# Performance work log

Hardware: AMD Instinct MI355X
Metric: run time of the kernel (lower is better)

Reference implementation:

```python
import jax, jax.numpy as jnp
import numpy as np

K = 50  # top-k causal instances (UC_MIL constructor)


def setup_inputs() -> dict:
    key = jax.random.key(0)
    k1, k2 = jax.random.split(key)
    X = jax.random.normal(k1, (8, 4096, 768), dtype=jnp.float32)
    # GCN layer weight: nn.Linear(768, 1, bias=False) -> weight shape (1, 768)
    W = jax.random.normal(k2, (1, 768), dtype=jnp.float32) * 0.02
    return {"X": X, "W": W}


def reference(X, W):
    # X: (B, N, D) bag of instance features; W: (1, D) GCN weight
    B, N, D = X.shape
    k = K

    # --- build_adjacency_matrix, batched ---
    Xc = X - X.mean(axis=1, keepdims=True)                      # center over instances
    cov = jnp.einsum('bnd,bmd->bnm', Xc, Xc)                    # (B, N, N)
    var = jnp.sqrt(jnp.sum(Xc * Xc, axis=-1, keepdims=True)) + 1e-6  # (B, N, 1)
    corr = cov / (var * jnp.swapaxes(var, 1, 2))                # var @ var.T
    A = jnp.abs(corr)
    dinv = jnp.sum(A, axis=-1) ** (-0.5)                        # (B, N)
    # D @ A @ D with diagonal D == row/col scaling (same math, no dense diag)
    A_norm = dinv[:, :, None] * A * dinv[:, None, :]

    # --- 1-layer GCN score: (A_norm @ (X W^T)).squeeze(-1) ---
    XW = jnp.einsum('bnd,d->bn', X, W[0])                       # (B, N)
    S = jnp.einsum('bnm,bm->bn', A_norm, XW)                    # (B, N)

    # --- top-k causal / non-causal split, vectorized over batch ---
    _, topk_idx = jax.lax.top_k(S, k)                           # (B, k)
    F_c = jnp.take_along_axis(X, topk_idx[:, :, None], axis=1)  # (B, k, D)

    # non-topk indices in ascending order (torch.arange(N)[mask] semantics)
    flag = jnp.zeros((B, N), dtype=jnp.int32)
    flag = flag.at[jnp.arange(B)[:, None], topk_idx].set(1)
    non_idx = jnp.argsort(flag, axis=1, stable=True)[:, : N - k]  # (B, N-k)
    F_nc = jnp.take_along_axis(X, non_idx[:, :, None], axis=1)    # (B, N-k, D)

    # NOTE: original code has a bug: topk_indices = torch.stack(F_i_c, 0),
    # i.e. the second output is the gathered features, not the indices.
    # We replicate that faithfully.
    return (S,
            F_c,
            F_c.mean(axis=1, keepdims=True),
            F_nc.mean(axis=1, keepdims=True))
```

## Files before the change

kernel.cpp:

```cpp
#include <hip/hip_runtime.h>
#include <stdint.h>

typedef unsigned short u16;
typedef short bf16x8 __attribute__((ext_vector_type(8)));
typedef float f32x4 __attribute__((ext_vector_type(4)));
typedef unsigned long long ull;

#define NB 8
#define NROW 4096
#define ND 768
#define NKB 24
#define NRB 32
#define KTILE 4096
#define NTRI 528
#define TOPK 50

#define CPART_OFF 0u
#define CSUM_OFF  786432u
#define MEAN_OFF  811008u
#define RV_OFF    835584u
#define XW_OFF    966656u
#define T_OFF     1097728u
#define U_OFF     1228800u
#define IDX_OFF   1359872u
#define SMALL_TOTAL 1363968u
#define HB_PER_BATCH  6291456ull
#define COV_PER_BATCH 34603008ull
#define PER_BATCH (2ull * HB_PER_BATCH + COV_PER_BATCH)

static __device__ __forceinline__ u16 f2bf(float f) {
  uint32_t u = __float_as_uint(f);
  u += 0x7FFFu + ((u >> 16) & 1u);
  return (u16)(u >> 16);
}
static __device__ __forceinline__ float bf2f(u16 h) {
  return __uint_as_float(((uint32_t)h) << 16);
}

static __device__ __forceinline__ void gload_lds16(const char* g, char* l) {
  __builtin_amdgcn_global_load_lds(
      (const __attribute__((address_space(1))) uint32_t*)(const void*)g,
      (__attribute__((address_space(3))) uint32_t*)(void*)l, 16, 0, 0);
}

static __device__ __forceinline__ int tile_swz(int t) {
  return (t & 7) * 66 + (t >> 3);
}

__global__ __launch_bounds__(256)
void colsum1_kernel(const float* __restrict__ X, float* __restrict__ part) {
  const int nc = blockIdx.x;
  const int d  = threadIdx.x + blockIdx.y * 256;
  const int b  = blockIdx.z;
  const float* p = X + ((size_t)b * NROW + (size_t)nc * 128) * ND + d;
  float s = 0.f;
  for (int i = 0; i < 128; ++i) s += p[(size_t)i * ND];
  part[((size_t)b * 32 + nc) * ND + d] = s;
}

__global__ __launch_bounds__(256)
void colsum2_kernel(const float* __restrict__ part, float* __restrict__ csum,
                    float* __restrict__ mean) {
  const int d = threadIdx.x + blockIdx.x * 256;
  const int b = blockIdx.y;
  float s = 0.f;
  for (int i = 0; i < 32; ++i) s += part[((size_t)b * 32 + i) * ND + d];
  csum[(size_t)b * ND + d] = s;
  mean[(size_t)b * ND + d] = s * (1.0f / 4096.0f);
}

__global__ __launch_bounds__(128)
void rowstats_kernel(const float* __restrict__ X, const float* __restrict__ W,
                     const float* __restrict__ mean,
                     u16* __restrict__ hi, u16* __restrict__ lo,
                     float* __restrict__ rv, float* __restrict__ xw, int b0) {
  const int n  = blockIdx.x;
  const int lb = blockIdx.y;
  const int gb = b0 + lb;
  const int tid = threadIdx.x;
  const float* xr = X + ((size_t)gb * NROW + n) * ND;
  const float* mb = mean + (size_t)gb * ND;
  const int r = n & 127, rbk = n >> 7;
  float ssq = 0.f, sw = 0.f;
  if (tid < 96) {
    const int d0 = tid * 8;
    const float4 xa = *(const float4*)(xr + d0);
    const float4 xb = *(const float4*)(xr + d0 + 4);
    const float4 ma = *(const float4*)(mb + d0);
    const float4 mc = *(const float4*)(mb + d0 + 4);
    const float4 wa = *(const float4*)(W + d0);
    const float4 wb = *(const float4*)(W + d0 + 4);
    float x[8]  = {xa.x, xa.y, xa.z, xa.w, xb.x, xb.y, xb.z, xb.w};
    float mm[8] = {ma.x, ma.y, ma.z, ma.w, mc.x, mc.y, mc.z, mc.w};
    float ww[8] = {wa.x, wa.y, wa.z, wa.w, wb.x, wb.y, wb.z, wb.w};
    u16 hbits[8], lbits[8];
#pragma unroll
    for (int i = 0; i < 8; ++i) {
      float xc = x[i] - mm[i];
      ssq += xc * xc;
      sw  += x[i] * ww[i];
      u16 hb = f2bf(xc);
      float hf = bf2f(hb);
      u16 lb2 = f2bf(xc - hf);
      hbits[i] = hb; lbits[i] = lb2;
    }
    const int kb = d0 >> 5;
    const int kk = d0 & 31;
    const size_t tbyte = ((size_t)((lb * NRB + rbk) * NKB + kb)) * 8192
                       + (size_t)((r * 64 + kk * 2) ^ ((r & 7) << 4));
    uint4 hv, lv;
    hv.x = (uint32_t)hbits[0] | ((uint32_t)hbits[1] << 16);
    hv.y = (uint32_t)hbits[2] | ((uint32_t)hbits[3] << 16);
    hv.z = (uint32_t)hbits[4] | ((uint32_t)hbits[5] << 16);
    hv.w = (uint32_t)hbits[6] | ((uint32_t)hbits[7] << 16);
    lv.x = (uint32_t)lbits[0] | ((uint32_t)lbits[1] << 16);
    lv.y = (uint32_t)lbits[2] | ((uint32_t)lbits[3] << 16);
    lv.z = (uint32_t)lbits[4] | ((uint32_t)lbits[5] << 16);
    lv.w = (uint32_t)lbits[6] | ((uint32_t)lbits[7] << 16);
    *(uint4*)((char*)hi + tbyte) = hv;
    *(uint4*)((char*)lo + tbyte) = lv;
  }
#pragma unroll
  for (int m = 1; m < 64; m <<= 1) {
    ssq += __shfl_xor(ssq, m, 64);
    sw  += __shfl_xor(sw, m, 64);
  }
  __shared__ float sh[4];
  const int w = tid >> 6, lane = tid & 63;
  if (lane == 0) { sh[w * 2] = ssq; sh[w * 2 + 1] = sw; }
  __syncthreads();
  if (tid == 0) {
    float S = sh[0] + sh[2];
    float T = sh[1] + sh[3];
    const size_t i = (size_t)gb * NROW + n;
    rv[i] = 1.0f / (sqrtf(S) + 1e-6f);
    xw[i] = T;
  }
}

static __device__ __forceinline__ bf16x8 read_frag(const u16* sm, int r, int kbyte) {
  const int byte = (r * 64 + kbyte) ^ ((r & 7) << 4);
  return *(const bf16x8*)((const char*)sm + byte);
}

__global__ __launch_bounds__(256, 2)
void gemm_acc_kernel(const u16* __restrict__ hi, const u16* __restrict__ lo,
                     const float* __restrict__ coef, float* __restrict__ outacc,
                     float* __restrict__ covout, int b0) {
  const int lb = blockIdx.y;
  const int gb = b0 + lb;
  const int tsw = tile_swz(blockIdx.x);
  int trem = tsw;
  int rb = 0;
  while (trem >= NRB - rb) { trem -= NRB - rb; ++rb; }
  const int cb = rb + trem;

  __shared__ u16 sm[4 * KTILE];
  u16* aHi = sm;
  u16* bHi = sm + KTILE;
  u16* aLo = sm + 2 * KTILE;
  u16* bLo = sm + 3 * KTILE;

  const int tid = threadIdx.x;
  const int lane = tid & 63;
  const int wid = tid >> 6;
  const int wrow = wid >> 1, wcol = wid & 1;
  const int l15 = lane & 15, lg = lane >> 4;

  const char* hA = (const char*)(hi + (size_t)((lb * NRB + rb) * NKB) * KTILE);
  const char* hB = (const char*)(hi + (size_t)((lb * NRB + cb) * NKB) * KTILE);
  const char* lA = (const char*)(lo + (size_t)((lb * NRB + rb) * NKB) * KTILE);
  const char* lB = (const char*)(lo + (size_t)((lb * NRB + cb) * NKB) * KTILE);

  f32x4 acc[4][4];
#pragma unroll
  for (int i = 0; i < 4; ++i)
#pragma unroll
    for (int j = 0; j < 4; ++j) acc[i][j] = f32x4{0.f, 0.f, 0.f, 0.f};

  for (int kb = 0; kb < NKB; ++kb) {
    __syncthreads();
    const size_t kb8 = (size_t)kb * 8192;
#pragma unroll
    for (int it = 0; it < 2; ++it) {
      const int off = it * 4096 + tid * 16;
      gload_lds16(hA + kb8 + off, (char*)aHi + off);
      gload_lds16(hB + kb8 + off, (char*)bHi + off);
      gload_lds16(lA + kb8 + off, (char*)aLo + off);
      gload_lds16(lB + kb8 + off, (char*)bLo + off);
    }
    __syncthreads();

    bf16x8 ah[4], bh[4], al[4], bl[4];
#pragma unroll
    for (int i = 0; i < 4; ++i) {
      ah[i] = read_frag(aHi, wrow * 64 + i * 16 + l15, lg * 16);
      bh[i] = read_frag(bHi, wcol * 64 + i * 16 + l15, lg * 16);
      al[i] = read_frag(aLo, wrow * 64 + i * 16 + l15, lg * 16);
      bl[i] = read_frag(bLo, wcol * 64 + i * 16 + l15, lg * 16);
    }
#pragma unroll
    for (int mi = 0; mi < 4; ++mi)
#pragma unroll
      for (int ni = 0; ni < 4; ++ni) {
        acc[mi][ni] = __builtin_amdgcn_mfma_f32_16x16x32_bf16(ah[mi], bh[ni], acc[mi][ni], 0, 0, 0);
        acc[mi][ni] = __builtin_amdgcn_mfma_f32_16x16x32_bf16(ah[mi], bl[ni], acc[mi][ni], 0, 0, 0);
        acc[mi][ni] = __builtin_amdgcn_mfma_f32_16x16x32_bf16(al[mi], bh[ni], acc[mi][ni], 0, 0, 0);
      }
  }

  const float* cf = coef + (size_t)gb * NROW;
  float* oa = outacc + (size_t)gb * NROW;
  const int rbase = rb * 128 + wrow * 64;
  const int cbase = cb * 128 + wcol * 64;

  float* cv = covout + ((size_t)lb * NTRI + tsw) * 16384;
#pragma unroll
  for (int mi = 0; mi < 4; ++mi)
#pragma unroll
    for (int ni = 0; ni < 4; ++ni)
#pragma unroll
      for (int j = 0; j < 4; ++j)
        cv[(wrow * 64 + mi * 16 + lg * 4 + j) * 128 + wcol * 64 + ni * 16 + l15] =
            fabsf(acc[mi][ni][j]);

  float ccol[4];
#pragma unroll
  for (int ni = 0; ni < 4; ++ni) ccol[ni] = cf[cbase + ni * 16 + l15];

  float rs[4][4];
#pragma unroll
  for (int mi = 0; mi < 4; ++mi)
#pragma unroll
    for (int j = 0; j < 4; ++j) {
      float s = 0.f;
#pragma unroll
      for (int ni = 0; ni < 4; ++ni) s += fabsf(acc[mi][ni][j]) * ccol[ni];
      rs[mi][j] = s;
    }
#pragma unroll
  for (int m = 1; m < 16; m <<= 1)
#pragma unroll
    for (int mi = 0; mi < 4; ++mi)
#pragma unroll
      for (int j = 0; j < 4; ++j) rs[mi][j] += __shfl_xor(rs[mi][j], m, 64);
  if (l15 == 0) {
#pragma unroll
    for (int mi = 0; mi < 4; ++mi)
#pragma unroll
      for (int j = 0; j < 4; ++j)
        atomicAdd(&oa[rbase + mi * 16 + lg * 4 + j], rs[mi][j]);
  }

  if (rb != cb) {
    float crow[4][4];
#pragma unroll
    for (int mi = 0; mi < 4; ++mi)
#pragma unroll
      for (int j = 0; j < 4; ++j) crow[mi][j] = cf[rbase + mi * 16 + lg * 4 + j];
    float cs[4];
#pragma unroll
    for (int ni = 0; ni < 4; ++ni) {
      float s = 0.f;
#pragma unroll
      for (int mi = 0; mi < 4; ++mi)
#pragma unroll
        for (int j = 0; j < 4; ++j) s += fabsf(acc[mi][ni][j]) * crow[mi][j];
      cs[ni] = s;
    }
#pragma unroll
    for (int ni = 0; ni < 4; ++ni) {
      cs[ni] += __shfl_xor(cs[ni], 16, 64);
      cs[ni] += __shfl_xor(cs[ni], 32, 64);
    }
    if (lg == 0) {
#pragma unroll
      for (int ni = 0; ni < 4; ++ni)
        atomicAdd(&oa[cbase + ni * 16 + l15], cs[ni]);
    }
  }
}

__global__ __launch_bounds__(256)
void upass_kernel(const float* __restrict__ cov, const float* __restrict__ tt,
                  const float* __restrict__ rv, const float* __restrict__ xw,
                  float* __restrict__ uacc, int b0) {
  const int lb = blockIdx.y;
  const int gb = b0 + lb;
  const int tsw = tile_swz(blockIdx.x);
  int trem = tsw;
  int rb = 0;
  while (trem >= NRB - rb) { trem -= NRB - rb; ++rb; }
  const int cb = rb + trem;

  const float* A = cov + ((size_t)lb * NTRI + tsw) * 16384;
  const size_t bo = (size_t)gb * NROW;

  __shared__ float wr[128];
  __shared__ float rsum[128];
  __shared__ float csum_p[8][128];

  const int t = threadIdx.x;
  const int g = t >> 5;
  const int l = t & 31;

  if (t < 128) {
    const int row = rb * 128 + t;
    wr[t] = (1.0f / sqrtf(rv[bo + row] * tt[bo + row])) * xw[bo + row] * rv[bo + row];
  }
  float4 wc4;
  {
    const int col = cb * 128 + l * 4;
    const float4 r4 = *(const float4*)(rv + bo + col);
    const float4 t4 = *(const float4*)(tt + bo + col);
    const float4 x4 = *(const float4*)(xw + bo + col);
    wc4.x = (1.0f / sqrtf(r4.x * t4.x)) * x4.x * r4.x;
    wc4.y = (1.0f / sqrtf(r4.y * t4.y)) * x4.y * r4.y;
    wc4.z = (1.0f / sqrtf(r4.z * t4.z)) * x4.z * r4.z;
    wc4.w = (1.0f / sqrtf(r4.w * t4.w)) * x4.w * r4.w;
  }
  __syncthreads();

  float sc0 = 0.f, sc1 = 0.f, sc2 = 0.f, sc3 = 0.f;
#pragma unroll
  for (int i = 0; i < 16; ++i) {
    const int r = g + i * 8;
    const float4 v = *(const float4*)(A + r * 128 + l * 4);
    float p = v.x * wc4.x + v.y * wc4.y + v.z * wc4.z + v.w * wc4.w;
    const float wrr = wr[r];
    sc0 += v.x * wrr; sc1 += v.y * wrr; sc2 += v.z * wrr; sc3 += v.w * wrr;
#pragma unroll
    for (int m = 1; m < 32; m <<= 1) p += __shfl_xor(p, m, 64);
    if (l == 0) rsum[r] = p;
  }
  csum_p[g][l * 4 + 0] = sc0;
  csum_p[g][l * 4 + 1] = sc1;
  csum_p[g][l * 4 + 2] = sc2;
  csum_p[g][l * 4 + 3] = sc3;
  __syncthreads();

  float* ua = uacc + bo;
  if (t < 128) atomicAdd(&ua[rb * 128 + t], rsum[t]);
  if (rb != cb && t < 128) {
    float s = 0.f;
#pragma unroll
    for (int gg = 0; gg < 8; ++gg) s += csum_p[gg][t];
    atomicAdd(&ua[cb * 128 + t], s);
  }
}

__global__ __launch_bounds__(1024)
void topk_kernel(const float* __restrict__ tt, const float* __restrict__ rv,
                 const float* __restrict__ u, float* __restrict__ S,
                 int* __restrict__ idx) {
  const int b = blockIdx.x;
  __shared__ ull keys[NROW];
  __shared__ ull wred[16];
  const int t = threadIdx.x;
  const int lane = t & 63, w = t >> 6;
  const size_t bo = (size_t)b * NROW;
#pragma unroll
  for (int j = 0; j < 4; ++j) {
    const int i = t + j * 1024;
    const float rvi = rv[bo + i];
    const float s = (1.0f / sqrtf(rvi * tt[bo + i])) * rvi * u[bo + i];
    S[bo + i] = s;
    uint32_t uu = __float_as_uint(s);
    uu = (uu & 0x80000000u) ? ~uu : (uu | 0x80000000u);
    keys[i] = ((ull)uu << 32) | (uint32_t)(4095 - i);
  }
  __syncthreads();
  for (int r = 0; r < TOPK; ++r) {
    ull m = keys[t];
    ull m2 = keys[t + 1024]; if (m2 > m) m = m2;
    m2 = keys[t + 2048]; if (m2 > m) m = m2;
    m2 = keys[t + 3072]; if (m2 > m) m = m2;
#pragma unroll
    for (int sh = 1; sh < 64; sh <<= 1) {
      ull o = __shfl_xor(m, sh, 64);
      if (o > m) m = o;
    }
    if (lane == 0) wred[w] = m;
    __syncthreads();
    if (w == 0) {
      ull mm = wred[lane & 15];
#pragma unroll
      for (int sh = 1; sh < 16; sh <<= 1) {
        ull o = __shfl_xor(mm, sh, 64);
        if (o > mm) mm = o;
      }
      if (lane == 0) {
        const int sel = 4095 - (int)(mm & 0xFFFFFFFFu);
        idx[b * TOPK + r] = sel;
        keys[sel] = 0ULL;
      }
    }
    __syncthreads();
  }
}

__global__ __launch_bounds__(768)
void gathermeans_kernel(const float* __restrict__ X, const int* __restrict__ idx,
                        const float* __restrict__ csum, float* __restrict__ outFc,
                        float* __restrict__ outC, float* __restrict__ outNC) {
  const int b = blockIdx.x;
  const int d = threadIdx.x;
  float s = 0.f;
  for (int r = 0; r < TOPK; ++r) {
    const int row = idx[b * TOPK + r];
    const float v = X[((size_t)b * NROW + row) * ND + d];
    outFc[((size_t)b * TOPK + r) * ND + d] = v;
    s += v;
  }
  outC[(size_t)b * ND + d]  = s * (1.0f / 50.0f);
  outNC[(size_t)b * ND + d] = (csum[(size_t)b * ND + d] - s) * (1.0f / 4046.0f);
}

extern "C" void kernel_launch(void* const* d_in, const int* in_sizes, int n_in,
                              void* d_out, int out_size, void* d_ws, size_t ws_size,
                              hipStream_t stream) {
  const float* X = (const float*)d_in[0];
  const float* W = (const float*)d_in[1];
  float* out = (float*)d_out;
  char* ws = (char*)d_ws;

  float* cpart = (float*)(ws + CPART_OFF);
  float* csum  = (float*)(ws + CSUM_OFF);
  float* mean  = (float*)(ws + MEAN_OFF);
  float* rv    = (float*)(ws + RV_OFF);
  float* xw    = (float*)(ws + XW_OFF);
  float* tacc  = (float*)(ws + T_OFF);
  float* uacc  = (float*)(ws + U_OFF);
  int*   idx   = (int*)(ws + IDX_OFF);

  int nbc = 1;
  if (ws_size > SMALL_TOTAL + PER_BATCH)
    nbc = (int)((ws_size - SMALL_TOTAL) / PER_BATCH);
  if (nbc > NB) nbc = NB;
  if (nbc < 1) nbc = 1;
  u16* hi   = (u16*)(ws + SMALL_TOTAL);
  u16* lo   = (u16*)(ws + SMALL_TOTAL + (size_t)nbc * HB_PER_BATCH);
  float* cov = (float*)(ws + SMALL_TOTAL + (size_t)nbc * 2 * HB_PER_BATCH);

  float* outS  = out;
  float* outFc = out + 32768;
  float* outMC = out + 339968;
  float* outMN = out + 346112;

  hipMemsetAsync(ws + T_OFF, 0, 262144, stream);

  colsum1_kernel<<<dim3(32, 3, NB), 256, 0, stream>>>(X, cpart);
  colsum2_kernel<<<dim3(3, NB), 256, 0, stream>>>(cpart, csum, mean);

  for (int b0 = 0; b0 < NB; b0 += nbc) {
    const int nb = (NB - b0 < nbc) ? (NB - b0) : nbc;
    rowstats_kernel<<<dim3(NROW, nb), 128, 0, stream>>>(X, W, mean, hi, lo, rv, xw, b0);
    gemm_acc_kernel<<<dim3(NTRI, nb), 256, 0, stream>>>(hi, lo, rv, tacc, cov, b0);
    upass_kernel<<<dim3(NTRI, nb), 256, 0, stream>>>(cov, tacc, rv, xw, uacc, b0);
  }

  topk_kernel<<<NB, 1024, 0, stream>>>(tacc, rv, uacc, outS, idx);
  gathermeans_kernel<<<NB, 768, 0, stream>>>(X, idx, csum, outFc, outMC, outMN);
}
```

Baseline: 494.5 us.

## Enlarge GEMM tiles to 256x256 with double-buffered LDS and phased MFMA scheduling

The symmetric covariance GEMM moves from 128x128 tiles with 256 threads to 256x256 tiles with 512 threads, so far fewer triangular tiles are needed and each loaded operand is reused more. The LDS is now double-buffered: the next K slice is prefetched into the second buffer while the current one is consumed. MFMA work is split into barrier-separated phases with raised priority (setprio). The upass kernel is adapted to the larger tile layout. The cost is 128KB of LDS per block and 128 accumulator floats per thread, which lowers occupancy and leaves fewer blocks to fill the GPU.

```diff
diff --git a/kernel.cpp b/kernel.cpp
--- a/kernel.cpp
+++ b/kernel.cpp
@@ -12,7 +12,8 @@
 #define NKB 24
 #define NRB 32
 #define KTILE 4096
-#define NTRI 528
+#define NRB2 16
+#define NTRI2 136
 #define TOPK 50
 
 #define CPART_OFF 0u
@@ -25,7 +26,7 @@
 #define IDX_OFF   1359872u
 #define SMALL_TOTAL 1363968u
 #define HB_PER_BATCH  6291456ull
-#define COV_PER_BATCH 34603008ull
+#define COV_PER_BATCH 35651584ull
 #define PER_BATCH (2ull * HB_PER_BATCH + COV_PER_BATCH)
 
 static __device__ __forceinline__ u16 f2bf(float f) {
@@ -44,7 +45,7 @@
 }
 
 static __device__ __forceinline__ int tile_swz(int t) {
-  return (t & 7) * 66 + (t >> 3);
+  return (t & 7) * 17 + (t >> 3);
 }
 
 __global__ __launch_bounds__(256)
@@ -138,12 +139,27 @@
   }
 }
 
-static __device__ __forceinline__ bf16x8 read_frag(const u16* sm, int r, int kbyte) {
-  const int byte = (r * 64 + kbyte) ^ ((r & 7) << 4);
-  return *(const bf16x8*)((const char*)sm + byte);
-}
-
-__global__ __launch_bounds__(256, 2)
+static __device__ __forceinline__ bf16x8 rf(const char* region, int r, int kbyte) {
+  const int rr = r & 127;
+  const int byte = (r >> 7) * 8192 + ((rr * 64 + kbyte) ^ ((rr & 7) << 4));
+  return *(const bf16x8*)(region + byte);
+}
+
+#define STAGE(kb, dst) do { const size_t kof_ = (size_t)(kb) * 8192;      \
+  _Pragma("unroll") for (int i_ = 0; i_ < 8; ++i_)                         \
+    gload_lds16(gtile + kof_ + i_ * 1024, (dst) + i_ * 1024); } while (0)
+
+#define PHASE_MFMA(m0, aH0, aL0, aH1, aL1) do {                            \
+  _Pragma("unroll") for (int nf_ = 0; nf_ < 4; ++nf_) {                    \
+    acc[m0][nf_]     = __builtin_amdgcn_mfma_f32_16x16x32_bf16(aH0, bh[nf_], acc[m0][nf_], 0, 0, 0);     \
+    acc[m0][nf_]     = __builtin_amdgcn_mfma_f32_16x16x32_bf16(aH0, bl[nf_], acc[m0][nf_], 0, 0, 0);     \
+    acc[m0][nf_]     = __builtin_amdgcn_mfma_f32_16x16x32_bf16(aL0, bh[nf_], acc[m0][nf_], 0, 0, 0);     \
+    acc[(m0)+1][nf_] = __builtin_amdgcn_mfma_f32_16x16x32_bf16(aH1, bh[nf_], acc[(m0)+1][nf_], 0, 0, 0); \
+    acc[(m0)+1][nf_] = __builtin_amdgcn_mfma_f32_16x16x32_bf16(aH1, bl[nf_], acc[(m0)+1][nf_], 0, 0, 0); \
+    acc[(m0)+1][nf_] = __builtin_amdgcn_mfma_f32_16x16x32_bf16(aL1, bh[nf_], acc[(m0)+1][nf_], 0, 0, 0); \
+  } } while (0)
+
+__global__ __launch_bounds__(512, 2)
 void gemm_acc_kernel(const u16* __restrict__ hi, const u16* __restrict__ lo,
                      const float* __restrict__ coef, float* __restrict__ outacc,
                      float* __restrict__ covout, int b0) {
@@ -152,133 +168,153 @@
   const int tsw = tile_swz(blockIdx.x);
   int trem = tsw;
   int rb = 0;
-  while (trem >= NRB - rb) { trem -= NRB - rb; ++rb; }
+  while (trem >= NRB2 - rb) { trem -= NRB2 - rb; ++rb; }
   const int cb = rb + trem;
 
-  __shared__ u16 sm[4 * KTILE];
-  u16* aHi = sm;
-  u16* bHi = sm + KTILE;
-  u16* aLo = sm + 2 * KTILE;
-  u16* bLo = sm + 3 * KTILE;
+  __shared__ char sm[2][65536];
 
   const int tid = threadIdx.x;
   const int lane = tid & 63;
   const int wid = tid >> 6;
-  const int wrow = wid >> 1, wcol = wid & 1;
+  const int wr = wid >> 2, wc = wid & 3;
   const int l15 = lane & 15, lg = lane >> 4;
 
-  const char* hA = (const char*)(hi + (size_t)((lb * NRB + rb) * NKB) * KTILE);
-  const char* hB = (const char*)(hi + (size_t)((lb * NRB + cb) * NKB) * KTILE);
-  const char* lA = (const char*)(lo + (size_t)((lb * NRB + rb) * NKB) * KTILE);
-  const char* lB = (const char*)(lo + (size_t)((lb * NRB + cb) * NKB) * KTILE);
-
-  f32x4 acc[4][4];
-#pragma unroll
-  for (int i = 0; i < 4; ++i)
+  const int so = tid >> 7;
+  const int sh = (tid >> 6) & 1;
+  const int sl = tid & 63;
+  const u16* sarr = (so & 2) ? lo : hi;
+  const int  pb   = (so & 1) ? cb : rb;
+  const char* gtile = (const char*)(sarr + (size_t)((lb * NRB + (2 * pb + sh)) * NKB) * KTILE)
+                    + sl * 16;
+  char* ldst0 = &sm[0][0] + so * 16384 + sh * 8192 + sl * 16;
+  char* ldst1 = &sm[1][0] + so * 16384 + sh * 8192 + sl * 16;
+
+  f32x4 acc[8][4];
+#pragma unroll
+  for (int i = 0; i < 8; ++i)
 #pragma unroll
     for (int j = 0; j < 4; ++j) acc[i][j] = f32x4{0.f, 0.f, 0.f, 0.f};
 
+  STAGE(0, ldst0);
+
+  int cur = 0;
   for (int kb = 0; kb < NKB; ++kb) {
-    __syncthreads();
-    const size_t kb8 = (size_t)kb * 8192;
-#pragma unroll
-    for (int it = 0; it < 2; ++it) {
-      const int off = it * 4096 + tid * 16;
-      gload_lds16(hA + kb8 + off, (char*)aHi + off);
-      gload_lds16(hB + kb8 + off, (char*)bHi + off);
-      gload_lds16(lA + kb8 + off, (char*)aLo + off);
-      gload_lds16(lB + kb8 + off, (char*)bLo + off);
-    }
-    __syncthreads();
-
-    bf16x8 ah[4], bh[4], al[4], bl[4];
-#pragma unroll
-    for (int i = 0; i < 4; ++i) {
-      ah[i] = read_frag(aHi, wrow * 64 + i * 16 + l15, lg * 16);
-      bh[i] = read_frag(bHi, wcol * 64 + i * 16 + l15, lg * 16);
-      al[i] = read_frag(aLo, wrow * 64 + i * 16 + l15, lg * 16);
-      bl[i] = read_frag(bLo, wcol * 64 + i * 16 + l15, lg * 16);
-    }
-#pragma unroll
-    for (int mi = 0; mi < 4; ++mi)
-#pragma unroll
-      for (int ni = 0; ni < 4; ++ni) {
-        acc[mi][ni] = __builtin_amdgcn_mfma_f32_16x16x32_bf16(ah[mi], bh[ni], acc[mi][ni], 0, 0, 0);
-        acc[mi][ni] = __builtin_amdgcn_mfma_f32_16x16x32_bf16(ah[mi], bl[ni], acc[mi][ni], 0, 0, 0);
-        acc[mi][ni] = __builtin_amdgcn_mfma_f32_16x16x32_bf16(al[mi], bh[ni], acc[mi][ni], 0, 0, 0);
-      }
+    asm volatile("s_waitcnt vmcnt(0)" ::: "memory");
+    __builtin_amdgcn_s_barrier();
+    const char* smc = cur ? &sm[1][0] : &sm[0][0];
+    char* nxt = cur ? ldst0 : ldst1;
+    const char* aH = smc;
+    const char* bH = smc + 16384;
+    const char* aL = smc + 32768;
+    const char* bL = smc + 49152;
+
+    bf16x8 bh[4], bl[4];
+#pragma unroll
+    for (int nf = 0; nf < 4; ++nf) {
+      const int r = wc * 64 + nf * 16 + l15;
+      bh[nf] = rf(bH, r, lg * 16);
+      bl[nf] = rf(bL, r, lg * 16);
+    }
+    bf16x8 a0h = rf(aH, wr * 128 + 0 * 16 + l15, lg * 16);
+    bf16x8 a0l = rf(aL, wr * 128 + 0 * 16 + l15, lg * 16);
+    bf16x8 a1h = rf(aH, wr * 128 + 1 * 16 + l15, lg * 16);
+    bf16x8 a1l = rf(aL, wr * 128 + 1 * 16 + l15, lg * 16);
+    if (kb + 1 < NKB) { STAGE(kb + 1, nxt); }
+    __builtin_amdgcn_s_barrier();
+    __builtin_amdgcn_s_setprio(1);
+    PHASE_MFMA(0, a0h, a0l, a1h, a1l);
+    __builtin_amdgcn_s_setprio(0);
+    __builtin_amdgcn_s_barrier();
+
+#pragma unroll
+    for (int p = 1; p < 4; ++p) {
+      bf16x8 c0h = rf(aH, wr * 128 + (2 * p) * 16 + l15, lg * 16);
+      bf16x8 c0l = rf(aL, wr * 128 + (2 * p) * 16 + l15, lg * 16);
+      bf16x8 c1h = rf(aH, wr * 128 + (2 * p + 1) * 16 + l15, lg * 16);
+      bf16x8 c1l = rf(aL, wr * 128 + (2 * p + 1) * 16 + l15, lg * 16);
+      __builtin_amdgcn_s_barrier();
+      __builtin_amdgcn_s_setprio(1);
+      PHASE_MFMA(2 * p, c0h, c0l, c1h, c1l);
+      __builtin_amdgcn_s_setprio(0);
+      __builtin_amdgcn_s_barrier();
+    }
+    cur ^= 1;
   }
 
   const float* cf = coef + (size_t)gb * NROW;
   float* oa = outacc + (size_t)gb * NROW;
-  const int rbase = rb * 128 + wrow * 64;
-  const int cbase = cb * 128 + wcol * 64;
-
-  float* cv = covout + ((size_t)lb * NTRI + tsw) * 16384;
-#pragma unroll
-  for (int mi = 0; mi < 4; ++mi)
-#pragma unroll
-    for (int ni = 0; ni < 4; ++ni)
+  const int rbase = rb * 256 + wr * 128;
+  const int cbase = cb * 256 + wc * 64;
+
+  float* cv = covout + ((size_t)lb * NTRI2 + tsw) * 65536;
+#pragma unroll
+  for (int mf = 0; mf < 8; ++mf)
+#pragma unroll
+    for (int nf = 0; nf < 4; ++nf)
 #pragma unroll
       for (int j = 0; j < 4; ++j)
-        cv[(wrow * 64 + mi * 16 + lg * 4 + j) * 128 + wcol * 64 + ni * 16 + l15] =
-            fabsf(acc[mi][ni][j]);
+        cv[(size_t)(wr * 128 + mf * 16 + lg * 4 + j) * 256 + wc * 64 + nf * 16 + l15] =
+            fabsf(acc[mf][nf][j]);
 
   float ccol[4];
 #pragma unroll
-  for (int ni = 0; ni < 4; ++ni) ccol[ni] = cf[cbase + ni * 16 + l15];
-
-  float rs[4][4];
-#pragma unroll
-  for (int mi = 0; mi < 4; ++mi)
+  for (int nf = 0; nf < 4; ++nf) ccol[nf] = cf[cbase + nf * 16 + l15];
+
+#pragma unroll
+  for (int mf = 0; mf < 8; ++mf) {
+    float rs[4];
 #pragma unroll
     for (int j = 0; j < 4; ++j) {
       float s = 0.f;
 #pragma unroll
-      for (int ni = 0; ni < 4; ++ni) s += fabsf(acc[mi][ni][j]) * ccol[ni];
-      rs[mi][j] = s;
-    }
-#pragma unroll
-  for (int m = 1; m < 16; m <<= 1)
-#pragma unroll
-    for (int mi = 0; mi < 4; ++mi)
-#pragma unroll
-      for (int j = 0; j < 4; ++j) rs[mi][j] += __shfl_xor(rs[mi][j], m, 64);
-  if (l15 == 0) {
-#pragma unroll
-    for (int mi = 0; mi < 4; ++mi)
+      for (int nf = 0; nf < 4; ++nf) s += fabsf(acc[mf][nf][j]) * ccol[nf];
+      rs[j] = s;
+    }
+#pragma unroll
+    for (int m = 1; m < 16; m <<= 1)
+#pragma unroll
+      for (int j = 0; j < 4; ++j) rs[j] += __shfl_xor(rs[j], m, 64);
+    if (l15 == 0) {
 #pragma unroll
       for (int j = 0; j < 4; ++j)
-        atomicAdd(&oa[rbase + mi * 16 + lg * 4 + j], rs[mi][j]);
+        atomicAdd(&oa[rbase + mf * 16 + lg * 4 + j], rs[j]);
+    }
   }
 
   if (rb != cb) {
-    float crow[4][4];
-#pragma unroll
-    for (int mi = 0; mi < 4; ++mi)
-#pragma unroll
-      for (int j = 0; j < 4; ++j) crow[mi][j] = cf[rbase + mi * 16 + lg * 4 + j];
-    float cs[4];
-#pragma unroll
-    for (int ni = 0; ni < 4; ++ni) {
-      float s = 0.f;
-#pragma unroll
-      for (int mi = 0; mi < 4; ++mi)
-#pragma unroll
-        for (int j = 0; j < 4; ++j) s += fabsf(acc[mi][ni][j]) * crow[mi][j];
-      cs[ni] = s;
-    }
-#pragma unroll
-    for (int ni = 0; ni < 4; ++ni) {
-      cs[ni] += __shfl_xor(cs[ni], 16, 64);
-      cs[ni] += __shfl_xor(cs[ni], 32, 64);
+    float cs[4] = {0.f, 0.f, 0.f, 0.f};
+#pragma unroll
+    for (int mf = 0; mf < 8; ++mf)
+#pragma unroll
+      for (int j = 0; j < 4; ++j) {
+        const float cw = cf[rbase + mf * 16 + lg * 4 + j];
+#pragma unroll
+        for (int nf = 0; nf < 4; ++nf) cs[nf] += fabsf(acc[mf][nf][j]) * cw;
+      }
+#pragma unroll
+    for (int nf = 0; nf < 4; ++nf) {
+      cs[nf] += __shfl_xor(cs[nf], 16, 64);
+      cs[nf] += __shfl_xor(cs[nf], 32, 64);
     }
     if (lg == 0) {
 #pragma unroll
-      for (int ni = 0; ni < 4; ++ni)
-        atomicAdd(&oa[cbase + ni * 16 + l15], cs[ni]);
-    }
-  }
+      for (int nf = 0; nf < 4; ++nf)
+        atomicAdd(&oa[cbase + nf * 16 + l15], cs[nf]);
+    }
+  }
+}
+
+static __device__ __forceinline__ float4 wvec4(const float* rv, const float* tt,
+                                               const float* xw, size_t base) {
+  const float4 r4 = *(const float4*)(rv + base);
+  const float4 t4 = *(const float4*)(tt + base);
+  const float4 x4 = *(const float4*)(xw + base);
+  float4 o;
+  o.x = (1.0f / sqrtf(r4.x * t4.x)) * x4.x * r4.x;
+  o.y = (1.0f / sqrtf(r4.y * t4.y)) * x4.y * r4.y;
+  o.z = (1.0f / sqrtf(r4.z * t4.z)) * x4.z * r4.z;
+  o.w = (1.0f / sqrtf(r4.w * t4.w)) * x4.w * r4.w;
+  return o;
 }
 
 __global__ __launch_bounds__(256)
@@ -290,62 +326,61 @@
   const int tsw = tile_swz(blockIdx.x);
   int trem = tsw;
   int rb = 0;
-  while (trem >= NRB - rb) { trem -= NRB - rb; ++rb; }
+  while (trem >= NRB2 - rb) { trem -= NRB2 - rb; ++rb; }
   const int cb = rb + trem;
 
-  const float* A = cov + ((size_t)lb * NTRI + tsw) * 16384;
+  const float* A = cov + ((size_t)lb * NTRI2 + tsw) * 65536;
   const size_t bo = (size_t)gb * NROW;
 
-  __shared__ float wr[128];
-  __shared__ float rsum[128];
-  __shared__ float csum_p[8][128];
+  __shared__ float wr_[256];
+  __shared__ float rsum[256];
+  __shared__ float csum_p[8][256];
 
   const int t = threadIdx.x;
   const int g = t >> 5;
   const int l = t & 31;
 
-  if (t < 128) {
-    const int row = rb * 128 + t;
-    wr[t] = (1.0f / sqrtf(rv[bo + row] * tt[bo + row])) * xw[bo + row] * rv[bo + row];
-  }
-  float4 wc4;
   {
-    const int col = cb * 128 + l * 4;
-    const float4 r4 = *(const float4*)(rv + bo + col);
-    const float4 t4 = *(const float4*)(tt + bo + col);
-    const float4 x4 = *(const float4*)(xw + bo + col);
-    wc4.x = (1.0f / sqrtf(r4.x * t4.x)) * x4.x * r4.x;
-    wc4.y = (1.0f / sqrtf(r4.y * t4.y)) * x4.y * r4.y;
-    wc4.z = (1.0f / sqrtf(r4.z * t4.z)) * x4.z * r4.z;
-    wc4.w = (1.0f / sqrtf(r4.w * t4.w)) * x4.w * r4.w;
-  }
+    const int row = rb * 256 + t;
+    wr_[t] = (1.0f / sqrtf(rv[bo + row] * tt[bo + row])) * xw[bo + row] * rv[bo + row];
+  }
+  const float4 wcA = wvec4(rv, tt, xw, bo + cb * 256 + l * 4);
+  const float4 wcB = wvec4(rv, tt, xw, bo + cb * 256 + 128 + l * 4);
   __syncthreads();
 
-  float sc0 = 0.f, sc1 = 0.f, sc2 = 0.f, sc3 = 0.f;
-#pragma unroll
-  for (int i = 0; i < 16; ++i) {
+  float sA0 = 0.f, sA1 = 0.f, sA2 = 0.f, sA3 = 0.f;
+  float sB0 = 0.f, sB1 = 0.f, sB2 = 0.f, sB3 = 0.f;
+#pragma unroll 4
+  for (int i = 0; i < 32; ++i) {
     const int r = g + i * 8;
-    const float4 v = *(const float4*)(A + r * 128 + l * 4);
-    float p = v.x * wc4.x + v.y * wc4.y + v.z * wc4.z + v.w * wc4.w;
-    const float wrr = wr[r];
-    sc0 += v.x * wrr; sc1 += v.y * wrr; sc2 += v.z * wrr; sc3 += v.w * wrr;
+    const float4 vA = *(const float4*)(A + (size_t)r * 256 + l * 4);
+    const float4 vB = *(const float4*)(A + (size_t)r * 256 + 128 + l * 4);
+    float p = vA.x * wcA.x + vA.y * wcA.y + vA.z * wcA.z + vA.w * wcA.w
+            + vB.x * wcB.x + vB.y * wcB.y + vB.z * wcB.z + vB.w * wcB.w;
+    const float wrr = wr_[r];
+    sA0 += vA.x * wrr; sA1 += vA.y * wrr; sA2 += vA.z * wrr; sA3 += vA.w * wrr;
+    sB0 += vB.x * wrr; sB1 += vB.y * wrr; sB2 += vB.z * wrr; sB3 += vB.w * wrr;
 #pragma unroll
     for (int m = 1; m < 32; m <<= 1) p += __shfl_xor(p, m, 64);
     if (l == 0) rsum[r] = p;
   }
-  csum_p[g][l * 4 + 0] = sc0;
-  csum_p[g][l * 4 + 1] = sc1;
-  csum_p[g][l * 4 + 2] = sc2;
-  csum_p[g][l * 4 + 3] = sc3;
+  csum_p[g][l * 4 + 0] = sA0;
+  csum_p[g][l * 4 + 1] = sA1;
+  csum_p[g][l * 4 + 2] = sA2;
+  csum_p[g][l * 4 + 3] = sA3;
+  csum_p[g][128 + l * 4 + 0] = sB0;
+  csum_p[g][128 + l * 4 + 1] = sB1;
+  csum_p[g][128 + l * 4 + 2] = sB2;
+  csum_p[g][128 + l * 4 + 3] = sB3;
   __syncthreads();
 
   float* ua = uacc + bo;
-  if (t < 128) atomicAdd(&ua[rb * 128 + t], rsum[t]);
-  if (rb != cb && t < 128) {
+  atomicAdd(&ua[rb * 256 + t], rsum[t]);
+  if (rb != cb) {
     float s = 0.f;
 #pragma unroll
     for (int gg = 0; gg < 8; ++gg) s += csum_p[gg][t];
-    atomicAdd(&ua[cb * 128 + t], s);
+    atomicAdd(&ua[cb * 256 + t], s);
   }
 }
 
@@ -455,8 +490,8 @@
   for (int b0 = 0; b0 < NB; b0 += nbc) {
     const int nb = (NB - b0 < nbc) ? (NB - b0) : nbc;
     rowstats_kernel<<<dim3(NROW, nb), 128, 0, stream>>>(X, W, mean, hi, lo, rv, xw, b0);
-    gemm_acc_kernel<<<dim3(NTRI, nb), 256, 0, stream>>>(hi, lo, rv, tacc, cov, b0);
-    upass_kernel<<<dim3(NTRI, nb), 256, 0, stream>>>(cov, tacc, rv, xw, uacc, b0);
+    gemm_acc_kernel<<<dim3(NTRI2, nb), 512, 0, stream>>>(hi, lo, rv, tacc, cov, b0);
+    upass_kernel<<<dim3(NTRI2, nb), 256, 0, stream>>>(cov, tacc, rv, xw, uacc, b0);
   }
 
   topk_kernel<<<NB, 1024, 0, stream>>>(tacc, rv, uacc, outS, idx);
```

Result: slower. 547.4 us (+10.7%).
